# Kernel optimization log

Measured on AMD Instinct MI355X. Metric: run time of the kernel, lower is better.

## Reference

```python
import jax, jax.numpy as jnp
import numpy as np

Q, B, D = 512, 4, 1024      # qlen, batch, d_model
L, H, DH, DI = 4, 16, 64, 4096  # layers, heads, d_head, d_inner
M = 512                      # mem_len


def setup_inputs() -> dict:
    key = jax.random.key(0)
    ks = jax.random.split(key, 10)
    w = lambda i, shape: jax.random.normal(ks[i], shape, jnp.float32) * 0.02
    return dict(
        x=jax.random.normal(ks[0], (Q, B, D), jnp.float32),
        mems=jax.random.normal(ks[1], (L, M, B, D), jnp.float32),
        u=w(2, (H, DH)),
        v=w(3, (H, DH)),
        W_qkv=w(4, (L, D, 3 * H * DH)),
        W_o=w(5, (L, H * DH, D)),
        W_r=w(6, (L, D, H * DH)),
        ln1_g=jnp.ones((L, D), jnp.float32),
        ln1_b=jnp.zeros((L, D), jnp.float32),
        W1=w(7, (L, D, DI)),
        b1=jnp.zeros((L, DI), jnp.float32),
        W2=w(8, (L, DI, D)),
        b2=jnp.zeros((L, D), jnp.float32),
        ln2_g=jnp.ones((L, D), jnp.float32),
        ln2_b=jnp.zeros((L, D), jnp.float32),
    )


def _layer_norm(x, g, b):
    mu = x.mean(-1, keepdims=True)
    var = ((x - mu) ** 2).mean(-1, keepdims=True)
    return (x - mu) * jax.lax.rsqrt(var + 1e-5) * g + b


def _rel_shift(x):
    # x: [q, k, b, n] -> Transformer-XL relative shift
    q, k, b, n = x.shape
    x = jnp.pad(x, ((0, 0), (1, 0), (0, 0), (0, 0)))
    return x.reshape(k + 1, q, b, n)[1:].reshape(q, k, b, n)


def _pos_emb(klen, d):
    pos = jnp.arange(klen - 1, -1, -1.0, dtype=jnp.float32)
    inv_freq = 1.0 / (10000.0 ** (jnp.arange(0, d, 2, dtype=jnp.float32) / d))
    ang = pos[:, None] * inv_freq[None, :]
    return jnp.concatenate([jnp.sin(ang), jnp.cos(ang)], axis=-1)  # [klen, d]


def reference(x, mems, u, v, W_qkv, W_o, W_r, ln1_g, ln1_b, W1, b1, W2, b2, ln2_g, ln2_b):
    q_len, bsz, d = x.shape
    mlen = mems.shape[1]
    klen = mlen + q_len
    r = _pos_emb(klen, d)                       # [klen, d]
    scale = 1.0 / np.sqrt(DH)
    # causal mask with memory: query i may attend key j iff j - i <= mlen
    mask = (jnp.arange(klen)[None, :] - jnp.arange(q_len)[:, None]) > mlen  # [q, k]
    h = x
    for i in range(L):
        cat = jnp.concatenate([mems[i], h], axis=0)       # [klen, b, d]
        heads = cat @ W_qkv[i]                            # [klen, b, 3*H*DH]
        qh, kh, vh = jnp.split(heads, 3, axis=-1)
        qh = qh[-q_len:].reshape(q_len, bsz, H, DH)
        kh = kh.reshape(klen, bsz, H, DH)
        vh = vh.reshape(klen, bsz, H, DH)
        rk = (r @ W_r[i]).reshape(klen, H, DH)            # [klen, H, DH]
        AC = jnp.einsum('ibnd,jbnd->ijbn', qh + u, kh)
        BD = _rel_shift(jnp.einsum('ibnd,jnd->ijbn', qh + v, rk))
        score = (AC + BD) * scale                         # [q, k, b, n]
        score = jnp.where(mask[:, :, None, None], -1e30, score)
        attn = jax.nn.softmax(score, axis=1)
        av = jnp.einsum('ijbn,jbnd->ibnd', attn, vh).reshape(q_len, bsz, H * DH)
        h = _layer_norm(h + av @ W_o[i], ln1_g[i], ln1_b[i])
        ff = jax.nn.relu(h @ W1[i] + b1[i]) @ W2[i] + b2[i]
        h = _layer_norm(h + ff, ln2_g[i], ln2_b[i])
    return h  # [qlen, bsz, d_model]
```

## Files before the change

### kernel.cpp

```cpp
#include <hip/hip_runtime.h>
#include <hip/hip_bf16.h>
#include <cstdint>
#include <cmath>

#define QL      512
#define BS      4
#define DMODEL  1024
#define NL      4
#define NH      16
#define DHEAD   64
#define DINNER  4096
#define MLEN    512
#define KLEN_   1024
#define HD_     1024
#define THD     3072
#define ROWS_H   2048

typedef __attribute__((ext_vector_type(8))) __bf16 bf16x8;
typedef __attribute__((ext_vector_type(4))) __bf16 bf16x4;
typedef __attribute__((ext_vector_type(4))) float  f32x4;

enum EpiMode { EPI_F32 = 0, EPI_BF16 = 1, EPI_RELU_BF16 = 2 };

#define SCL 0.18033688011112042f

__device__ __forceinline__ void glds16(const void* g, void* l) {
  __builtin_amdgcn_global_load_lds(
      (const __attribute__((address_space(1))) unsigned int*)g,
      (__attribute__((address_space(3))) unsigned int*)l, 16, 0, 0);
}

template<int BM, int BN, int WMT, int WNT, int EPI>
__global__ __launch_bounds__(256) void gemm_bt(
    const __bf16* __restrict__ A, const __bf16* __restrict__ Bt,
    void* __restrict__ Cv, const float* __restrict__ bias,
    int K, int lda, int ldb, int ldc,
    long sA, long Bn, long Cn)
{
  constexpr int WCOLS = BN / (WNT * 16);
  constexpr int WROWS = BM / (WMT * 16);
  static_assert(WCOLS * WROWS == 4, "must be 4 waves");
  __shared__ __align__(16) char smem[(BM + BN) * 128];
  char* sA0 = smem;
  char* sA1 = smem + BM * 64;
  char* sB0 = smem + BM * 128;
  char* sB1 = smem + BM * 128 + BN * 64;

  const int bz = blockIdx.z;
  A  += (size_t)bz * sA;
  Bt += (size_t)bz * Bn;
  const size_t coff = (size_t)bz * Cn;

  const int tid  = threadIdx.x;
  const int wave = tid >> 6, lane = tid & 63;
  const int quad = lane >> 4, mrow = lane & 15;
  const int wr = wave / WCOLS, wc = wave % WCOLS;
  const int bm0 = blockIdx.x * BM, bn0 = blockIdx.y * BN;

  const int srow = lane >> 2;
  const int skq  = (lane & 3) ^ (srow & 3);
  const __bf16* gA = A  + (size_t)(bm0 + wave * (BM / 64) * 16 + srow) * lda + skq * 8;
  const __bf16* gB = Bt + (size_t)(bn0 + wave * (BN / 64) * 16 + srow) * ldb + skq * 8;
  char* lA0 = sA0 + wave * (BM / 64) * 1024;
  char* lA1 = sA1 + wave * (BM / 64) * 1024;
  char* lB0 = sB0 + wave * (BN / 64) * 1024;
  char* lB1 = sB1 + wave * (BN / 64) * 1024;

  const int aswz = (quad ^ (mrow & 3)) << 4;

  const f32x4 zero = {0.f, 0.f, 0.f, 0.f};
  f32x4 acc[WMT][WNT];
#pragma unroll
  for (int a = 0; a < WMT; ++a)
#pragma unroll
    for (int b = 0; b < WNT; ++b) acc[a][b] = zero;

  for (int k0 = 0; k0 < K; k0 += 64) {
#pragma unroll
    for (int p = 0; p < BM / 64; ++p) {
      glds16(gA + (size_t)p * 16 * lda + k0,      lA0 + p * 1024);
      glds16(gA + (size_t)p * 16 * lda + k0 + 32, lA1 + p * 1024);
    }
#pragma unroll
    for (int p = 0; p < BN / 64; ++p) {
      glds16(gB + (size_t)p * 16 * ldb + k0,      lB0 + p * 1024);
      glds16(gB + (size_t)p * 16 * ldb + k0 + 32, lB1 + p * 1024);
    }
    __syncthreads();
    bf16x8 afr[WMT], bfr[WNT];
#pragma unroll
    for (int mt = 0; mt < WMT; ++mt)
      afr[mt] = *(const bf16x8*)(sA0 + (wr * (WMT * 16) + mt * 16 + mrow) * 64 + aswz);
#pragma unroll
    for (int nt = 0; nt < WNT; ++nt)
      bfr[nt] = *(const bf16x8*)(sB0 + (wc * (WNT * 16) + nt * 16 + mrow) * 64 + aswz);
#pragma unroll
    for (int mt = 0; mt < WMT; ++mt)
#pragma unroll
      for (int nt = 0; nt < WNT; ++nt)
        acc[mt][nt] = __builtin_amdgcn_mfma_f32_16x16x32_bf16(afr[mt], bfr[nt], acc[mt][nt], 0, 0, 0);
#pragma unroll
    for (int mt = 0; mt < WMT; ++mt)
      afr[mt] = *(const bf16x8*)(sA1 + (wr * (WMT * 16) + mt * 16 + mrow) * 64 + aswz);
#pragma unroll
    for (int nt = 0; nt < WNT; ++nt)
      bfr[nt] = *(const bf16x8*)(sB1 + (wc * (WNT * 16) + nt * 16 + mrow) * 64 + aswz);
#pragma unroll
    for (int mt = 0; mt < WMT; ++mt)
#pragma unroll
      for (int nt = 0; nt < WNT; ++nt)
        acc[mt][nt] = __builtin_amdgcn_mfma_f32_16x16x32_bf16(afr[mt], bfr[nt], acc[mt][nt], 0, 0, 0);
    __syncthreads();
  }

#pragma unroll
  for (int mt = 0; mt < WMT; ++mt) {
#pragma unroll
    for (int nt = 0; nt < WNT; ++nt) {
#pragma unroll
      for (int rr = 0; rr < 4; ++rr) {
        int gm = bm0 + wr * (WMT * 16) + mt * 16 + quad * 4 + rr;
        int gn = bn0 + wc * (WNT * 16) + nt * 16 + mrow;
        float val = acc[mt][nt][rr];
        if constexpr (EPI == EPI_F32) {
          ((float*)Cv)[coff + (size_t)gm * ldc + gn] = val;
        } else if constexpr (EPI == EPI_BF16) {
          ((__bf16*)Cv)[coff + (size_t)gm * ldc + gn] = (__bf16)val;
        } else {
          val += bias[gn];
          ((__bf16*)Cv)[coff + (size_t)gm * ldc + gn] = (__bf16)fmaxf(val, 0.f);
        }
      }
    }
  }
}

__global__ __launch_bounds__(256) void flash_attn(
    const __bf16* __restrict__ qu,
    const __bf16* __restrict__ qv,
    const __bf16* __restrict__ heads,
    const __bf16* __restrict__ rk,
    const __bf16* __restrict__ vt,
    __bf16* __restrict__ avp,
    float* __restrict__ mlpart)
{
  __shared__ __align__(16) char kh_t[64 * 144];
  __shared__ __align__(16) char rv_t[64 * 144];
  __shared__ __align__(4) __bf16 rawb[64 * 134];

  const int wgid = blockIdx.x;
  const int xcd  = wgid & 7;
  const int slotw = wgid >> 3;
  const int bn   = ((slotw >> 4) << 3) + xcd;
  const int inner = slotw & 15;
  const int t    = 7 - (inner & 7);
  const int z    = inner >> 3;
  const int i0   = t * 64;
  const int b    = bn >> 4, n = bn & 15;
  const int nt   = t + 9;
  const int h    = (nt + 1) >> 1;
  const int ks   = z ? h : 0;
  const int ke   = z ? nt : h;

  const int tid = threadIdx.x;
  const int wave = tid >> 6, lane = tid & 63;
  const int quad = lane >> 4, mrow = lane & 15;
  const f32x4 zero = {0.f, 0.f, 0.f, 0.f};

  const __bf16* qub = qu + (size_t)bn * QL * DHEAD;
  const __bf16* qvb = qv + (size_t)bn * QL * DHEAD;
  const int qrow = i0 + wave * 16 + mrow;
  bf16x8 quf0 = *(const bf16x8*)(qub + (size_t)qrow * 64 + quad * 8);
  bf16x8 quf1 = *(const bf16x8*)(qub + (size_t)qrow * 64 + 32 + quad * 8);
  bf16x8 qvf0 = *(const bf16x8*)(qvb + (size_t)qrow * 64 + quad * 8);
  bf16x8 qvf1 = *(const bf16x8*)(qvb + (size_t)qrow * 64 + 32 + quad * 8);

  f32x4 o[4];
#pragma unroll
  for (int dt = 0; dt < 4; ++dt) o[dt] = zero;
  float m_r[4], l_r[4];
#pragma unroll
  for (int rr = 0; rr < 4; ++rr) { m_r[rr] = -3.0e38f; l_r[rr] = 0.f; }

  const int sr = tid >> 3;
  const int sc = (tid & 7) * 8;

  const __bf16* vtb = vt + (size_t)bn * (DHEAD * KLEN_);

  const int c0 = 448 - i0;
  const int cpre = c0 + 64 * ks;
#pragma unroll
  for (int p = 0; p < 2; ++p) {
    int r = p * 32 + sr;
    bf16x8 vv = *(const bf16x8*)(rk + (size_t)(cpre + r) * HD_ + n * 64 + sc);
    *(bf16x8*)(rv_t + r * 144 + sc * 2) = vv;
  }
  __syncthreads();
  {
    int slotc = ((cpre >> 6) & 1) * 64;
    __builtin_amdgcn_s_setprio(1);
#pragma unroll
    for (int ct = 0; ct < 4; ++ct) {
      bf16x8 b0 = *(const bf16x8*)(rv_t + (ct * 16 + mrow) * 144 + quad * 16);
      bf16x8 b1 = *(const bf16x8*)(rv_t + (ct * 16 + mrow) * 144 + 64 + quad * 16);
      f32x4 r = __builtin_amdgcn_mfma_f32_16x16x32_bf16(qvf0, b0, zero, 0, 0, 0);
      r = __builtin_amdgcn_mfma_f32_16x16x32_bf16(qvf1, b1, r, 0, 0, 0);
#pragma unroll
      for (int rr = 0; rr < 4; ++rr)
        rawb[(wave * 16 + quad * 4 + rr) * 134 + slotc + ct * 16 + mrow] = (__bf16)r[rr];
    }
    __builtin_amdgcn_s_setprio(0);
  }
  bf16x8 kreg0, kreg1, rreg0, rreg1, vreg0, vreg1;
  {
    int j0 = ks * 64;
    kreg0 = *(const bf16x8*)(heads + (size_t)((j0 + sr) * BS + b) * THD + HD_ + n * 64 + sc);
    kreg1 = *(const bf16x8*)(heads + (size_t)((j0 + 32 + sr) * BS + b) * THD + HD_ + n * 64 + sc);
    int c1 = c0 + 64 * (ks + 1);
    if (c1 < KLEN_) {
      rreg0 = *(const bf16x8*)(rk + (size_t)(c1 + sr) * HD_ + n * 64 + sc);
      rreg1 = *(const bf16x8*)(rk + (size_t)(c1 + 32 + sr) * HD_ + n * 64 + sc);
    }
  }
  __syncthreads();

  const int i_base = i0 + wave * 16 + quad * 4;
  for (int k = ks; k < ke; ++k) {
    const int j0 = k * 64;
    const int cw = c0 + 64 * (k + 1);
    vreg0 = *(const bf16x8*)(vtb + (size_t)sr * KLEN_ + j0 + sc);
    vreg1 = *(const bf16x8*)(vtb + (size_t)(32 + sr) * KLEN_ + j0 + sc);
    *(bf16x8*)(kh_t + sr * 144 + sc * 2) = kreg0;
    *(bf16x8*)(kh_t + (32 + sr) * 144 + sc * 2) = kreg1;
    if (cw < KLEN_) {
      *(bf16x8*)(rv_t + sr * 144 + sc * 2) = rreg0;
      *(bf16x8*)(rv_t + (32 + sr) * 144 + sc * 2) = rreg1;
    }
    __syncthreads();
    __builtin_amdgcn_s_setprio(1);
    if (cw < KLEN_) {
      int slotc = ((cw >> 6) & 1) * 64;
#pragma unroll
      for (int ct = 0; ct < 4; ++ct) {
        bf16x8 b0 = *(const bf16x8*)(rv_t + (ct * 16 + mrow) * 144 + quad * 16);
        bf16x8 b1 = *(const bf16x8*)(rv_t + (ct * 16 + mrow) * 144 + 64 + quad * 16);
        f32x4 r = __builtin_amdgcn_mfma_f32_16x16x32_bf16(qvf0, b0, zero, 0, 0, 0);
        r = __builtin_amdgcn_mfma_f32_16x16x32_bf16(qvf1, b1, r, 0, 0, 0);
#pragma unroll
        for (int rr = 0; rr < 4; ++rr)
          rawb[(wave * 16 + quad * 4 + rr) * 134 + slotc + ct * 16 + mrow] = (__bf16)r[rr];
      }
    }
    f32x4 s[4];
#pragma unroll
    for (int ct = 0; ct < 4; ++ct) {
      bf16x8 b0 = *(const bf16x8*)(kh_t + (ct * 16 + mrow) * 144 + quad * 16);
      bf16x8 b1 = *(const bf16x8*)(kh_t + (ct * 16 + mrow) * 144 + 64 + quad * 16);
      s[ct] = __builtin_amdgcn_mfma_f32_16x16x32_bf16(quf0, b0, zero, 0, 0, 0);
      s[ct] = __builtin_amdgcn_mfma_f32_16x16x32_bf16(quf1, b1, s[ct], 0, 0, 0);
    }
    __builtin_amdgcn_s_setprio(0);
    __syncthreads();
    if (k + 1 < ke) {
      int j1 = (k + 1) * 64;
      kreg0 = *(const bf16x8*)(heads + (size_t)((j1 + sr) * BS + b) * THD + HD_ + n * 64 + sc);
      kreg1 = *(const bf16x8*)(heads + (size_t)((j1 + 32 + sr) * BS + b) * THD + HD_ + n * 64 + sc);
      int cn2 = c0 + 64 * (k + 2);
      if (cn2 < KLEN_) {
        rreg0 = *(const bf16x8*)(rk + (size_t)(cn2 + sr) * HD_ + n * 64 + sc);
        rreg1 = *(const bf16x8*)(rk + (size_t)(cn2 + 32 + sr) * HD_ + n * 64 + sc);
      }
    }
    *(bf16x8*)(rv_t + sr * 144 + sc * 2) = vreg0;
    *(bf16x8*)(rv_t + (32 + sr) * 144 + sc * 2) = vreg1;
#pragma unroll
    for (int ct = 0; ct < 4; ++ct) {
#pragma unroll
      for (int rr = 0; rr < 4; ++rr) {
        int i = i_base + rr;
        int j = j0 + ct * 16 + mrow;
        float val;
        if (j - i <= MLEN) {
          int c = j - i + (QL - 1);
          int col = ((c >> 6) & 1) * 64 + (c & 63);
          val = (s[ct][rr] + (float)rawb[(wave * 16 + quad * 4 + rr) * 134 + col]) * SCL;
        } else val = -3.0e38f;
        s[ct][rr] = val;
      }
    }
    float alpha[4];
#pragma unroll
    for (int rr = 0; rr < 4; ++rr) {
      float mx = fmaxf(fmaxf(s[0][rr], s[1][rr]), fmaxf(s[2][rr], s[3][rr]));
#pragma unroll
      for (int off = 1; off < 16; off <<= 1) mx = fmaxf(mx, __shfl_xor(mx, off));
      float m_new = fmaxf(m_r[rr], mx);
      alpha[rr] = exp2f(m_r[rr] - m_new);
      m_r[rr] = m_new;
      float rs = 0.f;
#pragma unroll
      for (int ct = 0; ct < 4; ++ct) {
        float pv = exp2f(s[ct][rr] - m_new);
        s[ct][rr] = pv;
        rs += pv;
      }
#pragma unroll
      for (int off = 1; off < 16; off <<= 1) rs += __shfl_xor(rs, off);
      l_r[rr] = l_r[rr] * alpha[rr] + rs;
    }
#pragma unroll
    for (int dt = 0; dt < 4; ++dt)
#pragma unroll
      for (int rr = 0; rr < 4; ++rr) o[dt][rr] *= alpha[rr];
#pragma unroll
    for (int ct = 0; ct < 4; ++ct)
#pragma unroll
      for (int rr = 0; rr < 4; ++rr)
        ((__bf16*)kh_t)[(wave * 16 + quad * 4 + rr) * 72 + ct * 16 + mrow] = (__bf16)s[ct][rr];
    __syncthreads();
    {
      bf16x8 pf0 = *(const bf16x8*)(kh_t + (wave * 16 + mrow) * 144 + quad * 16);
      bf16x8 pf1 = *(const bf16x8*)(kh_t + (wave * 16 + mrow) * 144 + 64 + quad * 16);
      __builtin_amdgcn_s_setprio(1);
#pragma unroll
      for (int dt = 0; dt < 4; ++dt) {
        bf16x8 vf0 = *(const bf16x8*)(rv_t + (dt * 16 + mrow) * 144 + quad * 16);
        bf16x8 vf1 = *(const bf16x8*)(rv_t + (dt * 16 + mrow) * 144 + 64 + quad * 16);
        o[dt] = __builtin_amdgcn_mfma_f32_16x16x32_bf16(pf0, vf0, o[dt], 0, 0, 0);
        o[dt] = __builtin_amdgcn_mfma_f32_16x16x32_bf16(pf1, vf1, o[dt], 0, 0, 0);
      }
      __builtin_amdgcn_s_setprio(0);
    }
    __syncthreads();
  }

  const size_t prow = ((size_t)z * 64 + bn) * 512;
#pragma unroll
  for (int rr = 0; rr < 4; ++rr) {
    int i = i_base + rr;
    float inv = 1.0f / l_r[rr];
#pragma unroll
    for (int dt = 0; dt < 4; ++dt)
      avp[(prow + i) * 64 + dt * 16 + mrow] = (__bf16)(o[dt][rr] * inv);
  }
  if (mrow == 0) {
#pragma unroll
    for (int rr = 0; rr < 4; ++rr) {
      int i = i_base + rr;
      mlpart[(prow + i) * 2]     = m_r[rr];
      mlpart[(prow + i) * 2 + 1] = l_r[rr];
    }
  }
}

__global__ __launch_bounds__(256) void attn_combine(
    const __bf16* __restrict__ avp, const float* __restrict__ mlpart,
    __bf16* __restrict__ av)
{
  int idx = blockIdx.x * 256 + threadIdx.x;
  int dq = idx & 15;
  int i  = (idx >> 4) & 511;
  int bn = idx >> 13;
  int b = bn >> 4, n = bn & 15;
  size_t r0 = (size_t)bn * 512 + i;
  size_t r1 = r0 + (size_t)64 * 512;
  float m1 = mlpart[r0 * 2], l1 = mlpart[r0 * 2 + 1];
  float m2 = mlpart[r1 * 2], l2 = mlpart[r1 * 2 + 1];
  float m  = fmaxf(m1, m2);
  float w1 = l1 * exp2f(m1 - m), w2 = l2 * exp2f(m2 - m);
  float inv = 1.0f / (w1 + w2);
  w1 *= inv; w2 *= inv;
  bf16x4 o1 = *(const bf16x4*)(avp + r0 * 64 + dq * 4);
  bf16x4 o2 = *(const bf16x4*)(avp + r1 * 64 + dq * 4);
  bf16x4 ov;
#pragma unroll
  for (int j = 0; j < 4; ++j)
    ov[j] = (__bf16)((float)o1[j] * w1 + (float)o2[j] * w2);
  *(bf16x4*)(av + ((size_t)i * BS + b) * HD_ + n * 64 + dq * 4) = ov;
}


__global__ __launch_bounds__(256) void transpose_f32_bf16(
    const float* __restrict__ in, unsigned short* __restrict__ out, int R, int C)
{
  __shared__ float tile[64][66];
  int c0 = blockIdx.x * 64, r0 = blockIdx.y * 64;
  int tx = threadIdx.x, ty = threadIdx.y;
#pragma unroll
  for (int s = 0; s < 8; ++s) {
    int r = ty + s * 8;
    const float* p = in + (size_t)(r0 + r) * C + c0 + 2 * tx;
    tile[r][2 * tx]     = p[0];
    tile[r][2 * tx + 1] = p[1];
  }
  __syncthreads();
#pragma unroll
  for (int s = 0; s < 8; ++s) {
    int c = ty + s * 8;
    __bf16 lo = (__bf16)tile[2 * tx][c];
    __bf16 hi = (__bf16)tile[2 * tx + 1][c];
    unsigned int w = (unsigned int)*(unsigned short*)&lo |
                     ((unsigned int)*(unsigned short*)&hi << 16);
    *(unsigned int*)(out + (size_t)(c0 + c) * R + r0 + 2 * tx) = w;
  }
}

__global__ __launch_bounds__(256) void cast_f32_bf16(const float* __restrict__ in,
                                                     __bf16* __restrict__ out, int n)
{
  int i = blockIdx.x * 256 + threadIdx.x;
  if (i < n) out[i] = (__bf16)in[i];
}

__global__ __launch_bounds__(256) void posemb_kernel(__bf16* __restrict__ r)
{
  int idx = blockIdx.x * 256 + threadIdx.x;
  int p = idx >> 10, c = idx & 1023;
  int t = c & 511;
  float invf = __expf(-((float)t / 512.0f) * 9.210340371976184f);
  float ang = (float)(KLEN_ - 1 - p) * invf;
  float val = (c < 512) ? sinf(ang) : cosf(ang);
  r[idx] = (__bf16)val;
}

__global__ __launch_bounds__(256) void init_h(const float* __restrict__ x,
                                              float* __restrict__ hm,
                                              __bf16* __restrict__ hbf, int n)
{
  int i = blockIdx.x * 256 + threadIdx.x;
  if (i < n) { float t = x[i]; hm[i] = t; hbf[i] = (__bf16)t; }
}

__global__ __launch_bounds__(256) void build_quqv(const __bf16* __restrict__ heads,
                                                  const float* __restrict__ u,
                                                  const float* __restrict__ v,
                                                  __bf16* __restrict__ qu,
                                                  __bf16* __restrict__ qv)
{
  int idx = blockIdx.x * 256 + threadIdx.x;
  int d = idx & 63;
  int i = (idx >> 6) & (QL - 1);
  int bn = idx >> 15;
  int b = bn >> 4, n = bn & 15;
  float q = (float)heads[(size_t)((MLEN + i) * BS + b) * THD + n * 64 + d];
  int ud = n * 64 + d;
  qu[idx] = (__bf16)(q + u[ud]);
  qv[idx] = (__bf16)(q + v[ud]);
}

__global__ __launch_bounds__(256) void build_vt(const unsigned short* __restrict__ heads,
                                                unsigned short* __restrict__ vt)
{
  __shared__ unsigned short tile[64][65];
  int bn = blockIdx.y; int b = bn >> 4, n = bn & 15;
  int j0 = blockIdx.x * 64;
  int tx = threadIdx.x, ty = threadIdx.y;
#pragma unroll
  for (int s = 0; s < 16; ++s) {
    int j = ty + s * 4;
    tile[j][tx] = heads[(size_t)((j0 + j) * BS + b) * THD + 2048 + n * 64 + tx];
  }
  __syncthreads();
#pragma unroll
  for (int s = 0; s < 16; ++s) {
    int d = ty + s * 4;
    vt[(size_t)bn * DHEAD * KLEN_ + (size_t)d * KLEN_ + j0 + tx] = tile[tx][d];
  }
}

__global__ __launch_bounds__(256) void ln_kernel(float* __restrict__ hm,
                                                 const float* __restrict__ d0,
                                                 const float* __restrict__ d1,
                                                 const float* __restrict__ bias,
                                                 const float* __restrict__ g,
                                                 const float* __restrict__ b,
                                                 __bf16* __restrict__ hbf,
                                                 float* __restrict__ outf)
{
  int row = blockIdx.x;
  size_t base = (size_t)row * DMODEL;
  int tid = threadIdx.x;
  float x[4]; float sum = 0.f, sq = 0.f;
#pragma unroll
  for (int p = 0; p < 4; ++p) {
    int c = p * 256 + tid;
    float t = hm[base + c] + d0[base + c];
    if (d1) t += d1[base + c];
    if (bias) t += bias[c];
    x[p] = t; sum += t; sq += t * t;
  }
#pragma unroll
  for (int off = 32; off > 0; off >>= 1) { sum += __shfl_xor(sum, off); sq += __shfl_xor(sq, off); }
  __shared__ float rs[4], rq[4];
  int wave = tid >> 6, lane = tid & 63;
  if (lane == 0) { rs[wave] = sum; rq[wave] = sq; }
  __syncthreads();
  sum = rs[0] + rs[1] + rs[2] + rs[3];
  sq  = rq[0] + rq[1] + rq[2] + rq[3];
  float mu  = sum * (1.0f / DMODEL);
  float var = sq * (1.0f / DMODEL) - mu * mu;
  float rstd = rsqrtf(var + 1e-5f);
#pragma unroll
  for (int p = 0; p < 4; ++p) {
    int c = p * 256 + tid;
    float y = (x[p] - mu) * rstd * g[c] + b[c];
    hm[base + c] = y;
    hbf[base + c] = (__bf16)y;
    if (outf) outf[base + c] = y;
  }
}

extern "C" void kernel_launch(void* const* d_in, const int* in_sizes, int n_in,
                              void* d_out, int out_size, void* d_ws, size_t ws_size,
                              hipStream_t stream) {
  (void)in_sizes; (void)n_in; (void)out_size; (void)ws_size;
  const float* x    = (const float*)d_in[0];
  const float* mems = (const float*)d_in[1];
  const float* u    = (const float*)d_in[2];
  const float* v    = (const float*)d_in[3];
  const float* Wqkv = (const float*)d_in[4];
  const float* Wo   = (const float*)d_in[5];
  const float* Wr   = (const float*)d_in[6];
  const float* ln1g = (const float*)d_in[7];
  const float* ln1b = (const float*)d_in[8];
  const float* W1   = (const float*)d_in[9];
  const float* b1   = (const float*)d_in[10];
  const float* W2   = (const float*)d_in[11];
  const float* b2   = (const float*)d_in[12];
  const float* ln2g = (const float*)d_in[13];
  const float* ln2b = (const float*)d_in[14];

  size_t off = 0;
  char* ws = (char*)d_ws;
  auto alloc = [&](size_t bytes) { size_t o = off; off += (bytes + 255) & ~(size_t)255; return o; };
  __bf16* wT    = (__bf16*)(ws + alloc((size_t)DINNER * DMODEL * 2));
  char*   R1    = (char*)(ws + alloc((size_t)(2 * ROWS_H) * THD * 2));
  __bf16* heads = (__bf16*)R1;
  float*  proj  = (float*)R1;
  __bf16* ff1   = (__bf16*)(R1 + (size_t)ROWS_H * DMODEL * 4);
  __bf16* catb  = (__bf16*)(ws + alloc((size_t)(2 * ROWS_H) * DMODEL * 2));
  __bf16* memsb = catb;
  __bf16* hbf   = catb + (size_t)ROWS_H * DMODEL;
  __bf16* av    = catb;
  float*  mlprt = (float*)hbf;
  __bf16* avp   = wT;
  __bf16* r_bf  = (__bf16*)(ws + alloc((size_t)KLEN_ * DMODEL * 2));
  __bf16* rk4   = (__bf16*)(ws + alloc((size_t)NL * KLEN_ * HD_ * 2));
  __bf16* qu    = (__bf16*)(ws + alloc((size_t)2 * BS * NH * QL * DHEAD * 2));
  __bf16* qv    = qu + (size_t)BS * NH * QL * DHEAD;
  float*  ff2p  = (float*)qu;
  __bf16* vt    = (__bf16*)(ws + alloc((size_t)BS * NH * DHEAD * KLEN_ * 2));
  float*  hm    = (float*)(ws + alloc((size_t)ROWS_H * DMODEL * 4));

  posemb_kernel<<<(KLEN_ * DMODEL) / 256, 256, 0, stream>>>(r_bf);
  init_h<<<(ROWS_H * DMODEL) / 256, 256, 0, stream>>>(x, hm, hbf, ROWS_H * DMODEL);

  for (int i = 0; i < NL; ++i)
    transpose_f32_bf16<<<dim3(HD_ / 64, DMODEL / 64), dim3(32, 8), 0, stream>>>(
        Wr + (size_t)i * DMODEL * HD_, (unsigned short*)(wT + (size_t)i * HD_ * DMODEL),
        DMODEL, HD_);
  gemm_bt<128, 128, 4, 4, EPI_BF16><<<dim3(8, 8, NL), 256, 0, stream>>>(
      r_bf, wT, rk4, nullptr, DMODEL, DMODEL, DMODEL, HD_,
      0, (long)HD_ * DMODEL, (long)KLEN_ * HD_);

  for (int i = 0; i < NL; ++i) {
    cast_f32_bf16<<<(MLEN * BS * DMODEL) / 256, 256, 0, stream>>>(
        mems + (size_t)i * MLEN * BS * DMODEL, memsb, MLEN * BS * DMODEL);
    transpose_f32_bf16<<<dim3(THD / 64, DMODEL / 64), dim3(32, 8), 0, stream>>>(
        Wqkv + (size_t)i * DMODEL * THD, (unsigned short*)wT, DMODEL, THD);
    gemm_bt<128, 128, 4, 4, EPI_BF16><<<dim3(32, 24, 1), 256, 0, stream>>>(
        catb, wT, heads, nullptr, DMODEL, DMODEL, DMODEL, THD, 0, 0, 0);

    build_quqv<<<(BS * NH * QL * DHEAD) / 256, 256, 0, stream>>>(heads, u, v, qu, qv);
    build_vt<<<dim3(KLEN_ / 64, BS * NH), dim3(64, 4), 0, stream>>>(
        (const unsigned short*)heads, (unsigned short*)vt);

    flash_attn<<<dim3(1024), 256, 0, stream>>>(
        qu, qv, heads, rk4 + (size_t)i * KLEN_ * HD_, vt, avp, mlprt);
    attn_combine<<<(64 * 512 * 16) / 256, 256, 0, stream>>>(avp, mlprt, av);

    transpose_f32_bf16<<<dim3(DMODEL / 64, HD_ / 64), dim3(32, 8), 0, stream>>>(
        Wo + (size_t)i * HD_ * DMODEL, (unsigned short*)wT, HD_, DMODEL);
    gemm_bt<128, 64, 4, 2, EPI_F32><<<dim3(16, 16, 1), 256, 0, stream>>>(
        av, wT, proj, nullptr, HD_, HD_, HD_, DMODEL, 0, 0, 0);
    ln_kernel<<<ROWS_H, 256, 0, stream>>>(hm, proj, nullptr, nullptr,
                                          ln1g + i * DMODEL, ln1b + i * DMODEL, hbf, nullptr);

    transpose_f32_bf16<<<dim3(DINNER / 64, DMODEL / 64), dim3(32, 8), 0, stream>>>(
        W1 + (size_t)i * DMODEL * DINNER, (unsigned short*)wT, DMODEL, DINNER);
    gemm_bt<128, 128, 4, 4, EPI_RELU_BF16><<<dim3(16, 32, 1), 256, 0, stream>>>(
        hbf, wT, ff1, b1 + i * DINNER, DMODEL, DMODEL, DMODEL, DINNER, 0, 0, 0);

    transpose_f32_bf16<<<dim3(DMODEL / 64, DINNER / 64), dim3(32, 8), 0, stream>>>(
        W2 + (size_t)i * DINNER * DMODEL, (unsigned short*)wT, DINNER, DMODEL);
    gemm_bt<128, 64, 4, 2, EPI_F32><<<dim3(16, 16, 2), 256, 0, stream>>>(
        ff1, wT, proj, nullptr, DINNER / 2, DINNER, DINNER, DMODEL,
        (long)(DINNER / 2), (long)(DINNER / 2), (long)(ff2p - proj));
    ln_kernel<<<ROWS_H, 256, 0, stream>>>(hm, proj, ff2p, b2 + i * DMODEL,
                                          ln2g + i * DMODEL, ln2b + i * DMODEL, hbf,
                                          (i == NL - 1) ? (float*)d_out : nullptr);
  }
}
```

Measured before the change: 1.132 ms.

## Load K, R and V MFMA operands directly from global memory, drop LDS staging

The flash attention kernel no longer stages K, R and V tiles through shared memory with register prefetch. Each wave now loads its MFMA B operands straight from global memory. All block-wide barriers in the loop are replaced by per-wave lgkmcnt waits, since each wave only touches its own rows of the rawb and P buffers. This removes LDS traffic and synchronisation cost, but each wave now issues redundant, less coalesced global loads (strided rows of 16 bytes) with no software prefetch, so it leans on cache hits to hide latency.

```diff
diff --git a/kernel.cpp b/kernel.cpp
--- a/kernel.cpp
+++ b/kernel.cpp
@@ -144,8 +144,7 @@
     __bf16* __restrict__ avp,
     float* __restrict__ mlpart)
 {
-  __shared__ __align__(16) char kh_t[64 * 144];
-  __shared__ __align__(16) char rv_t[64 * 144];
+  __shared__ __align__(16) char p_t[64 * 144];
   __shared__ __align__(4) __bf16 rawb[64 * 134];
 
   const int wgid = blockIdx.x;
@@ -182,97 +181,68 @@
 #pragma unroll
   for (int rr = 0; rr < 4; ++rr) { m_r[rr] = -3.0e38f; l_r[rr] = 0.f; }
 
-  const int sr = tid >> 3;
-  const int sc = (tid & 7) * 8;
-
-  const __bf16* vtb = vt + (size_t)bn * (DHEAD * KLEN_);
+  const size_t kstride = (size_t)BS * THD;
+  const __bf16* kbase = heads + (size_t)b * THD + HD_ + n * 64 + quad * 8;
+  const __bf16* rbase = rk + n * 64 + quad * 8;
+  const __bf16* vbase = vt + (size_t)bn * (DHEAD * KLEN_)
+                      + (size_t)mrow * KLEN_ + quad * 8;
 
   const int c0 = 448 - i0;
-  const int cpre = c0 + 64 * ks;
-#pragma unroll
-  for (int p = 0; p < 2; ++p) {
-    int r = p * 32 + sr;
-    bf16x8 vv = *(const bf16x8*)(rk + (size_t)(cpre + r) * HD_ + n * 64 + sc);
-    *(bf16x8*)(rv_t + r * 144 + sc * 2) = vv;
-  }
-  __syncthreads();
+  const int rawrow = wave * 16 + quad * 4;
+
   {
-    int slotc = ((cpre >> 6) & 1) * 64;
-    __builtin_amdgcn_s_setprio(1);
+    const int cpre = c0 + 64 * ks;
+    const int slotc = ((cpre >> 6) & 1) * 64;
 #pragma unroll
     for (int ct = 0; ct < 4; ++ct) {
-      bf16x8 b0 = *(const bf16x8*)(rv_t + (ct * 16 + mrow) * 144 + quad * 16);
-      bf16x8 b1 = *(const bf16x8*)(rv_t + (ct * 16 + mrow) * 144 + 64 + quad * 16);
+      const __bf16* rp = rbase + (size_t)(cpre + ct * 16 + mrow) * HD_;
+      bf16x8 b0 = *(const bf16x8*)rp;
+      bf16x8 b1 = *(const bf16x8*)(rp + 32);
       f32x4 r = __builtin_amdgcn_mfma_f32_16x16x32_bf16(qvf0, b0, zero, 0, 0, 0);
       r = __builtin_amdgcn_mfma_f32_16x16x32_bf16(qvf1, b1, r, 0, 0, 0);
 #pragma unroll
       for (int rr = 0; rr < 4; ++rr)
-        rawb[(wave * 16 + quad * 4 + rr) * 134 + slotc + ct * 16 + mrow] = (__bf16)r[rr];
-    }
-    __builtin_amdgcn_s_setprio(0);
-  }
-  bf16x8 kreg0, kreg1, rreg0, rreg1, vreg0, vreg1;
-  {
-    int j0 = ks * 64;
-    kreg0 = *(const bf16x8*)(heads + (size_t)((j0 + sr) * BS + b) * THD + HD_ + n * 64 + sc);
-    kreg1 = *(const bf16x8*)(heads + (size_t)((j0 + 32 + sr) * BS + b) * THD + HD_ + n * 64 + sc);
-    int c1 = c0 + 64 * (ks + 1);
-    if (c1 < KLEN_) {
-      rreg0 = *(const bf16x8*)(rk + (size_t)(c1 + sr) * HD_ + n * 64 + sc);
-      rreg1 = *(const bf16x8*)(rk + (size_t)(c1 + 32 + sr) * HD_ + n * 64 + sc);
-    }
-  }
-  __syncthreads();
+        rawb[(rawrow + rr) * 134 + slotc + ct * 16 + mrow] = (__bf16)r[rr];
+    }
+  }
 
   const int i_base = i0 + wave * 16 + quad * 4;
   for (int k = ks; k < ke; ++k) {
     const int j0 = k * 64;
     const int cw = c0 + 64 * (k + 1);
-    vreg0 = *(const bf16x8*)(vtb + (size_t)sr * KLEN_ + j0 + sc);
-    vreg1 = *(const bf16x8*)(vtb + (size_t)(32 + sr) * KLEN_ + j0 + sc);
-    *(bf16x8*)(kh_t + sr * 144 + sc * 2) = kreg0;
-    *(bf16x8*)(kh_t + (32 + sr) * 144 + sc * 2) = kreg1;
-    if (cw < KLEN_) {
-      *(bf16x8*)(rv_t + sr * 144 + sc * 2) = rreg0;
-      *(bf16x8*)(rv_t + (32 + sr) * 144 + sc * 2) = rreg1;
-    }
-    __syncthreads();
     __builtin_amdgcn_s_setprio(1);
     if (cw < KLEN_) {
-      int slotc = ((cw >> 6) & 1) * 64;
+      const int slotc = ((cw >> 6) & 1) * 64;
 #pragma unroll
       for (int ct = 0; ct < 4; ++ct) {
-        bf16x8 b0 = *(const bf16x8*)(rv_t + (ct * 16 + mrow) * 144 + quad * 16);
-        bf16x8 b1 = *(const bf16x8*)(rv_t + (ct * 16 + mrow) * 144 + 64 + quad * 16);
+        const __bf16* rp = rbase + (size_t)(cw + ct * 16 + mrow) * HD_;
+        bf16x8 b0 = *(const bf16x8*)rp;
+        bf16x8 b1 = *(const bf16x8*)(rp + 32);
         f32x4 r = __builtin_amdgcn_mfma_f32_16x16x32_bf16(qvf0, b0, zero, 0, 0, 0);
         r = __builtin_amdgcn_mfma_f32_16x16x32_bf16(qvf1, b1, r, 0, 0, 0);
 #pragma unroll
         for (int rr = 0; rr < 4; ++rr)
-          rawb[(wave * 16 + quad * 4 + rr) * 134 + slotc + ct * 16 + mrow] = (__bf16)r[rr];
+          rawb[(rawrow + rr) * 134 + slotc + ct * 16 + mrow] = (__bf16)r[rr];
       }
     }
     f32x4 s[4];
 #pragma unroll
     for (int ct = 0; ct < 4; ++ct) {
-      bf16x8 b0 = *(const bf16x8*)(kh_t + (ct * 16 + mrow) * 144 + quad * 16);
-      bf16x8 b1 = *(const bf16x8*)(kh_t + (ct * 16 + mrow) * 144 + 64 + quad * 16);
+      const __bf16* kp = kbase + (size_t)(j0 + ct * 16 + mrow) * kstride;
+      bf16x8 b0 = *(const bf16x8*)kp;
+      bf16x8 b1 = *(const bf16x8*)(kp + 32);
       s[ct] = __builtin_amdgcn_mfma_f32_16x16x32_bf16(quf0, b0, zero, 0, 0, 0);
       s[ct] = __builtin_amdgcn_mfma_f32_16x16x32_bf16(quf1, b1, s[ct], 0, 0, 0);
     }
     __builtin_amdgcn_s_setprio(0);
-    __syncthreads();
-    if (k + 1 < ke) {
-      int j1 = (k + 1) * 64;
-      kreg0 = *(const bf16x8*)(heads + (size_t)((j1 + sr) * BS + b) * THD + HD_ + n * 64 + sc);
-      kreg1 = *(const bf16x8*)(heads + (size_t)((j1 + 32 + sr) * BS + b) * THD + HD_ + n * 64 + sc);
-      int cn2 = c0 + 64 * (k + 2);
-      if (cn2 < KLEN_) {
-        rreg0 = *(const bf16x8*)(rk + (size_t)(cn2 + sr) * HD_ + n * 64 + sc);
-        rreg1 = *(const bf16x8*)(rk + (size_t)(cn2 + 32 + sr) * HD_ + n * 64 + sc);
-      }
-    }
-    *(bf16x8*)(rv_t + sr * 144 + sc * 2) = vreg0;
-    *(bf16x8*)(rv_t + (32 + sr) * 144 + sc * 2) = vreg1;
+    bf16x8 vf0[4], vf1[4];
+#pragma unroll
+    for (int dt = 0; dt < 4; ++dt) {
+      const __bf16* vp = vbase + (size_t)(dt * 16) * KLEN_ + j0;
+      vf0[dt] = *(const bf16x8*)vp;
+      vf1[dt] = *(const bf16x8*)(vp + 32);
+    }
+    asm volatile("s_waitcnt lgkmcnt(0)" ::: "memory");
 #pragma unroll
     for (int ct = 0; ct < 4; ++ct) {
 #pragma unroll
@@ -283,7 +253,7 @@
         if (j - i <= MLEN) {
           int c = j - i + (QL - 1);
           int col = ((c >> 6) & 1) * 64 + (c & 63);
-          val = (s[ct][rr] + (float)rawb[(wave * 16 + quad * 4 + rr) * 134 + col]) * SCL;
+          val = (s[ct][rr] + (float)rawb[(rawrow + rr) * 134 + col]) * SCL;
         } else val = -3.0e38f;
         s[ct][rr] = val;
       }
@@ -316,22 +286,19 @@
     for (int ct = 0; ct < 4; ++ct)
 #pragma unroll
       for (int rr = 0; rr < 4; ++rr)
-        ((__bf16*)kh_t)[(wave * 16 + quad * 4 + rr) * 72 + ct * 16 + mrow] = (__bf16)s[ct][rr];
-    __syncthreads();
+        ((__bf16*)p_t)[(rawrow + rr) * 72 + ct * 16 + mrow] = (__bf16)s[ct][rr];
+    asm volatile("s_waitcnt lgkmcnt(0)" ::: "memory");
     {
-      bf16x8 pf0 = *(const bf16x8*)(kh_t + (wave * 16 + mrow) * 144 + quad * 16);
-      bf16x8 pf1 = *(const bf16x8*)(kh_t + (wave * 16 + mrow) * 144 + 64 + quad * 16);
+      bf16x8 pf0 = *(const bf16x8*)(p_t + (wave * 16 + mrow) * 144 + quad * 16);
+      bf16x8 pf1 = *(const bf16x8*)(p_t + (wave * 16 + mrow) * 144 + 64 + quad * 16);
       __builtin_amdgcn_s_setprio(1);
 #pragma unroll
       for (int dt = 0; dt < 4; ++dt) {
-        bf16x8 vf0 = *(const bf16x8*)(rv_t + (dt * 16 + mrow) * 144 + quad * 16);
-        bf16x8 vf1 = *(const bf16x8*)(rv_t + (dt * 16 + mrow) * 144 + 64 + quad * 16);
-        o[dt] = __builtin_amdgcn_mfma_f32_16x16x32_bf16(pf0, vf0, o[dt], 0, 0, 0);
-        o[dt] = __builtin_amdgcn_mfma_f32_16x16x32_bf16(pf1, vf1, o[dt], 0, 0, 0);
+        o[dt] = __builtin_amdgcn_mfma_f32_16x16x32_bf16(pf0, vf0[dt], o[dt], 0, 0, 0);
+        o[dt] = __builtin_amdgcn_mfma_f32_16x16x32_bf16(pf1, vf1[dt], o[dt], 0, 0, 0);
       }
       __builtin_amdgcn_s_setprio(0);
     }
-    __syncthreads();
   }
 
   const size_t prow = ((size_t)z * 64 + bn) * 512;
```

New measurement: 1.269 ms. 1.12x slower.
